# Kernel tuning notes

Hardware: AMD Instinct MI355X
Metric: run time of the kernel (lower is better)

## Reference

```python
import jax, jax.numpy as jnp
import numpy as np

B, N_IN, D_IN, N_OUT, D_OUT = 64, 2048, 16, 64, 16
GATE_EPS = 1e-6
SCALE = 1.0 / np.sqrt(D_OUT).astype(np.float32)  # 1/sqrt(out_d_capsules)


def setup_inputs() -> dict:
    key = jax.random.key(0)
    k0, k1, k2, k3, k4 = jax.random.split(key, 5)
    w_init = np.float32(np.sqrt(N_OUT / (D_IN * N_IN)))
    return {
        "input": jax.random.normal(k0, (B, N_IN, D_IN), jnp.float32),
        "current_act": jax.random.uniform(k1, (B, N_IN), jnp.float32),
        "next_capsule_value": jax.random.normal(k2, (B, N_OUT, D_OUT), jnp.float32),
        "next_act": jax.random.uniform(k3, (B, N_OUT), jnp.float32),
        "w": w_init * jax.random.normal(k4, (N_IN, D_IN, N_OUT, D_OUT), jnp.float32),
        "num_iter": 1,
    }


def reference(input, current_act, next_capsule_value, next_act, w, num_iter):
    # gate: gate_temp=1.0, gate_min=0, gate_max=1 -> reduces to clamp to [eps, 1-eps]
    act = jnp.clip(current_act, GATE_EPS, 1.0 - GATE_EPS)  # [B,N]
    # votes: shared between score and combine einsums (faithful: same contraction)
    votes = jnp.einsum('bna,namd->bnmd', input, w)  # [B,N,M,D]
    # routing logits: 'bna,namd,bmd->bnm' * scale
    scores = jnp.einsum('bnmd,bmd->bnm', votes, next_capsule_value) * SCALE
    qk = jax.nn.softmax(scores, axis=2)                       # softmax over out-capsules
    qk = qk * next_act[:, None, :]                            # 'bnm,bm->bnm'
    qk = qk / (jnp.sum(qk, axis=2, keepdims=True) + 1e-10)    # renormalize over m
    # combine: 'bnm,bna,namd,bn->bmd'
    out = jnp.einsum('bnm,bn,bnmd->bmd', qk, act, votes)      # [B,M,D]
    # act_type='EM' -> next_act passes through; dropout p=0 and identity nonlinearity
    return (out, next_act, qk)
```

## Files before the change

### kernel.cpp

```cpp
#include <hip/hip_runtime.h>
#include <stdint.h>
#include <stddef.h>

constexpr int B_ = 64, N_ = 2048, A_ = 16, M_ = 64, D_ = 16;
constexpr float SCALE_ = 0.25f;
constexpr float EPS_ = 1e-6f;

typedef float f32x4 __attribute__((ext_vector_type(4)));

#define GL16(g, l)                                                             \
  __builtin_amdgcn_global_load_lds((__attribute__((address_space(1))) void*)(g), \
                                   (__attribute__((address_space(3))) void*)(l), \
                                   16, 0, 0)

__global__ __launch_bounds__(256, 2)
void caps_main(
    const float* __restrict__ input,
    const float* __restrict__ cact,
    const float* __restrict__ ncv,
    const float* __restrict__ nact,
    const float* __restrict__ w,
    float* __restrict__ qk_out,
    float* __restrict__ partial,
    int C, int nch)
{
  __shared__ __align__(128) char wl[32768];

  const int tid  = threadIdx.x;
  const int lane = tid & 63;
  const int wv   = __builtin_amdgcn_readfirstlane(tid >> 6);

  const int flat = blockIdx.x;
  int bg, ch;
  if (nch & 7) { bg = flat & 3; ch = flat >> 2; }
  else { bg = (flat >> 3) & 3; ch = ((flat >> 5) << 3) | (flat & 7); }

  const int b0 = bg * 16 + wv * 4;
  const int n0 = ch * C;

  int offj[4];
#pragma unroll
  for (int j = 0; j < 4; ++j)
    offj[j] = (lane * 64 + j * 16) ^ (((lane >> 1) & 7) << 4);

  float na[4], cv[4][16];
#pragma unroll
  for (int bi = 0; bi < 4; ++bi) {
    na[bi] = nact[(b0 + bi) * M_ + lane];
    const f32x4* np4 = (const f32x4*)(ncv + ((size_t)(b0 + bi) * M_ + lane) * D_);
#pragma unroll
    for (int j = 0; j < 4; ++j) {
      const f32x4 t = np4[j];
      cv[bi][4*j+0] = t.x; cv[bi][4*j+1] = t.y;
      cv[bi][4*j+2] = t.z; cv[bi][4*j+3] = t.w;
    }
  }

  float acc[4][16];
#pragma unroll
  for (int bi = 0; bi < 4; ++bi)
#pragma unroll
    for (int d = 0; d < 16; ++d) acc[bi][d] = 0.f;

  for (int k = 0; k < C; ++k) {
    const int n = n0 + k;

    float v[4][16];
#pragma unroll
    for (int bi = 0; bi < 4; ++bi)
#pragma unroll
      for (int d = 0; d < 16; ++d) v[bi][d] = 0.f;

    int ibase[4];
#pragma unroll
    for (int bi = 0; bi < 4; ++bi)
      ibase[bi] = __builtin_amdgcn_readfirstlane(((b0 + bi) * N_ + n) * A_);

#pragma unroll
    for (int h = 0; h < 2; ++h) {
      {
        const char* ws = (const char*)w + ((size_t)n << 16) + ((size_t)h << 15);
#pragma unroll
        for (int i = 0; i < 8; ++i) {
          const uint32_t P = (uint32_t)(i * 4096 + tid * 16);
          const uint32_t S = P ^ (((P >> 7) & 7u) << 4);
          GL16(ws + S, (char*)wl + i * 4096 + wv * 1024);
        }
      }
      __syncthreads();

#pragma unroll
      for (int al = 0; al < 8; ++al) {
        f32x4 wr[4];
#pragma unroll
        for (int j = 0; j < 4; ++j)
          wr[j] = *(const f32x4*)((const char*)wl + al * 4096 + offj[j]);
#pragma unroll
        for (int bi = 0; bi < 4; ++bi) {
          const float x = input[ibase[bi] + h * 8 + al];
#pragma unroll
          for (int j = 0; j < 4; ++j) {
            v[bi][4*j+0] += x * wr[j].x; v[bi][4*j+1] += x * wr[j].y;
            v[bi][4*j+2] += x * wr[j].z; v[bi][4*j+3] += x * wr[j].w;
          }
        }
      }
      __syncthreads();
    }

#pragma unroll
    for (int bi = 0; bi < 4; ++bi) {
      float s = 0.f;
#pragma unroll
      for (int d = 0; d < 16; ++d) s += v[bi][d] * cv[bi][d];
      s *= SCALE_;
      const float e = __expf(s);
      const float ena = e * na[bi];
      float Ps = ena;
#pragma unroll
      for (int off = 32; off >= 1; off >>= 1) Ps += __shfl_xor(Ps, off, 64);
      const float qk = ena / Ps;
      qk_out[((size_t)(b0 + bi) * N_ + n) * M_ + lane] = qk;
      float ab = cact[__builtin_amdgcn_readfirstlane((b0 + bi) * N_ + n)];
      ab = fminf(fmaxf(ab, EPS_), 1.0f - EPS_);
      const float wq = qk * ab;
#pragma unroll
      for (int d = 0; d < 16; ++d) acc[bi][d] += wq * v[bi][d];
    }
  }

#pragma unroll
  for (int bi = 0; bi < 4; ++bi) {
    float* pp = partial + (((size_t)ch * B_ + (b0 + bi)) * M_ + lane) * D_;
#pragma unroll
    for (int j = 0; j < 4; ++j) {
      f32x4 t;
      t.x = acc[bi][4*j+0]; t.y = acc[bi][4*j+1];
      t.z = acc[bi][4*j+2]; t.w = acc[bi][4*j+3];
      __builtin_nontemporal_store(t, (f32x4*)pp + j);
    }
  }
}

__global__ void caps_reduce(const float* __restrict__ part,
                            const float* __restrict__ nain,
                            float* __restrict__ out, int nch)
{
  const int i = blockIdx.x * 256 + threadIdx.x;
  float s = 0.f;
  for (int c = 0; c < nch; ++c) s += part[(size_t)c * (B_ * M_ * D_) + i];
  out[i] = s;
  if (i < B_ * M_) out[B_ * M_ * D_ + i] = nain[i];
}

extern "C" void kernel_launch(void* const* d_in, const int* in_sizes, int n_in,
                              void* d_out, int out_size, void* d_ws, size_t ws_size,
                              hipStream_t stream)
{
  const float* input = (const float*)d_in[0];
  const float* cact  = (const float*)d_in[1];
  const float* ncv   = (const float*)d_in[2];
  const float* nact  = (const float*)d_in[3];
  const float* w     = (const float*)d_in[4];

  float* out     = (float*)d_out;
  float* qk_out  = out + (B_ * M_ * D_) + (B_ * M_);
  float* partial = (float*)d_ws;

  int nch = 256;
  while ((size_t)nch * (size_t)(B_ * M_ * D_) * sizeof(float) > ws_size && nch > 8) nch >>= 1;
  const int C = N_ / nch;

  hipLaunchKernelGGL(caps_main, dim3(4 * nch), dim3(256), 0, stream,
                     input, cact, ncv, nact, w, qk_out, partial, C, nch);
  hipLaunchKernelGGL(caps_reduce, dim3(B_ * M_ * D_ / 256), dim3(256), 0, stream,
                     partial, nact, out, nch);
}
```

Measured before the change: 217.1 us.

## Double-buffer weight tiles in LDS with manual vmcnt waits to overlap loads

Splits the weight staging into two 32KB LDS buffers. The next half-tile is issued via global_load_lds while the current one is computed, and explicit s_waitcnt vmcnt counts and barriers sequence the pipeline. Input values are now read as vectorized f32x4 loads per half instead of scalar loads inside the inner loop, and initial loads are drained up front. This roughly doubles LDS use to 64KB per block, which may limit occupancy at 2 blocks/CU, and the hand-counted vmcnt values must stay consistent with the issued loads.

```diff
diff --git a/kernel.cpp b/kernel.cpp
--- a/kernel.cpp
+++ b/kernel.cpp
@@ -12,6 +12,14 @@
   __builtin_amdgcn_global_load_lds((__attribute__((address_space(1))) void*)(g), \
                                    (__attribute__((address_space(3))) void*)(l), \
                                    16, 0, 0)
+
+#define WV(n) asm volatile("s_waitcnt vmcnt(" #n ")" ::: "memory")
+#define BAR() do {                        \
+    asm volatile("" ::: "memory");        \
+    __builtin_amdgcn_s_barrier();         \
+    asm volatile("" ::: "memory");        \
+    __builtin_amdgcn_sched_barrier(0);    \
+  } while (0)
 
 __global__ __launch_bounds__(256, 2)
 void caps_main(
@@ -24,7 +32,7 @@
     float* __restrict__ partial,
     int C, int nch)
 {
-  __shared__ __align__(128) char wl[32768];
+  __shared__ __align__(128) char wl[2][32768];
 
   const int tid  = threadIdx.x;
   const int lane = tid & 63;
@@ -55,6 +63,17 @@
       cv[bi][4*j+2] = t.z; cv[bi][4*j+3] = t.w;
     }
   }
+  {
+    float pin = 0.f;
+#pragma unroll
+    for (int bi = 0; bi < 4; ++bi) {
+      pin += na[bi];
+#pragma unroll
+      for (int d = 0; d < 16; ++d) pin += cv[bi][d];
+    }
+    asm volatile("" :: "v"(pin));
+    asm volatile("s_waitcnt vmcnt(0) lgkmcnt(0)" ::: "memory");
+  }
 
   float acc[4][16];
 #pragma unroll
@@ -62,72 +81,89 @@
 #pragma unroll
     for (int d = 0; d < 16; ++d) acc[bi][d] = 0.f;
 
-  for (int k = 0; k < C; ++k) {
-    const int n = n0 + k;
-
-    float v[4][16];
-#pragma unroll
-    for (int bi = 0; bi < 4; ++bi)
-#pragma unroll
-      for (int d = 0; d < 16; ++d) v[bi][d] = 0.f;
-
-    int ibase[4];
-#pragma unroll
-    for (int bi = 0; bi < 4; ++bi)
-      ibase[bi] = __builtin_amdgcn_readfirstlane(((b0 + bi) * N_ + n) * A_);
-
-#pragma unroll
-    for (int h = 0; h < 2; ++h) {
-      {
-        const char* ws = (const char*)w + ((size_t)n << 16) + ((size_t)h << 15);
-#pragma unroll
-        for (int i = 0; i < 8; ++i) {
-          const uint32_t P = (uint32_t)(i * 4096 + tid * 16);
-          const uint32_t S = P ^ (((P >> 7) & 7u) << 4);
-          GL16(ws + S, (char*)wl + i * 4096 + wv * 1024);
+  auto STAGE = [&](int h) {
+    const int n = n0 + (h >> 1);
+    const char* ws = (const char*)w + ((size_t)n << 16) + ((size_t)(h & 1) << 15);
+    char* lb = (char*)wl[h & 1] + wv * 1024;
+#pragma unroll
+    for (int i = 0; i < 8; ++i) {
+      const uint32_t P = (uint32_t)(i * 4096 + tid * 16);
+      const uint32_t S = P ^ (((P >> 7) & 7u) << 4);
+      GL16(ws + S, lb + i * 4096);
+    }
+  };
+
+  float v[4][16];
+
+  auto COMPUTE = [&](int h) {
+    const int n  = n0 + (h >> 1);
+    const int ah = h & 1;
+    const char* lb = (const char*)wl[ah];
+    if (ah == 0) {
+#pragma unroll
+      for (int bi = 0; bi < 4; ++bi)
+#pragma unroll
+        for (int d = 0; d < 16; ++d) v[bi][d] = 0.f;
+    }
+    float ib[4][8];
+#pragma unroll
+    for (int bi = 0; bi < 4; ++bi) {
+      const int ibase = __builtin_amdgcn_readfirstlane(
+          ((b0 + bi) * N_ + n) * A_ + ah * 8);
+      const f32x4 r0 = *(const f32x4*)(input + ibase);
+      const f32x4 r1 = *(const f32x4*)(input + ibase + 4);
+      ib[bi][0] = r0.x; ib[bi][1] = r0.y; ib[bi][2] = r0.z; ib[bi][3] = r0.w;
+      ib[bi][4] = r1.x; ib[bi][5] = r1.y; ib[bi][6] = r1.z; ib[bi][7] = r1.w;
+    }
+#pragma unroll
+    for (int al = 0; al < 8; ++al) {
+      f32x4 wr[4];
+#pragma unroll
+      for (int j = 0; j < 4; ++j)
+        wr[j] = *(const f32x4*)(lb + al * 4096 + offj[j]);
+#pragma unroll
+      for (int bi = 0; bi < 4; ++bi) {
+        const float x = ib[bi][al];
+#pragma unroll
+        for (int j = 0; j < 4; ++j) {
+          v[bi][4*j+0] += x * wr[j].x; v[bi][4*j+1] += x * wr[j].y;
+          v[bi][4*j+2] += x * wr[j].z; v[bi][4*j+3] += x * wr[j].w;
         }
       }
-      __syncthreads();
-
-#pragma unroll
-      for (int al = 0; al < 8; ++al) {
-        f32x4 wr[4];
-#pragma unroll
-        for (int j = 0; j < 4; ++j)
-          wr[j] = *(const f32x4*)((const char*)wl + al * 4096 + offj[j]);
-#pragma unroll
-        for (int bi = 0; bi < 4; ++bi) {
-          const float x = input[ibase[bi] + h * 8 + al];
-#pragma unroll
-          for (int j = 0; j < 4; ++j) {
-            v[bi][4*j+0] += x * wr[j].x; v[bi][4*j+1] += x * wr[j].y;
-            v[bi][4*j+2] += x * wr[j].z; v[bi][4*j+3] += x * wr[j].w;
-          }
-        }
+    }
+    if (ah == 1) {
+#pragma unroll
+      for (int bi = 0; bi < 4; ++bi) {
+        float s = 0.f;
+#pragma unroll
+        for (int d = 0; d < 16; ++d) s += v[bi][d] * cv[bi][d];
+        s *= SCALE_;
+        const float e = __expf(s);
+        const float ena = e * na[bi];
+        float Ps = ena;
+#pragma unroll
+        for (int off = 32; off >= 1; off >>= 1) Ps += __shfl_xor(Ps, off, 64);
+        const float qk = ena / Ps;
+        qk_out[((size_t)(b0 + bi) * N_ + n) * M_ + lane] = qk;
+        float ab = cact[__builtin_amdgcn_readfirstlane((b0 + bi) * N_ + n)];
+        ab = fminf(fmaxf(ab, EPS_), 1.0f - EPS_);
+        const float wq = qk * ab;
+#pragma unroll
+        for (int d = 0; d < 16; ++d) acc[bi][d] += wq * v[bi][d];
       }
-      __syncthreads();
-    }
-
-#pragma unroll
-    for (int bi = 0; bi < 4; ++bi) {
-      float s = 0.f;
-#pragma unroll
-      for (int d = 0; d < 16; ++d) s += v[bi][d] * cv[bi][d];
-      s *= SCALE_;
-      const float e = __expf(s);
-      const float ena = e * na[bi];
-      float Ps = ena;
-#pragma unroll
-      for (int off = 32; off >= 1; off >>= 1) Ps += __shfl_xor(Ps, off, 64);
-      const float qk = ena / Ps;
-      qk_out[((size_t)(b0 + bi) * N_ + n) * M_ + lane] = qk;
-      float ab = cact[__builtin_amdgcn_readfirstlane((b0 + bi) * N_ + n)];
-      ab = fminf(fmaxf(ab, EPS_), 1.0f - EPS_);
-      const float wq = qk * ab;
-#pragma unroll
-      for (int d = 0; d < 16; ++d) acc[bi][d] += wq * v[bi][d];
-    }
-  }
+    }
+  };
+
+  STAGE(0);
+  STAGE(1);
+  WV(8);  BAR(); COMPUTE(0); BAR(); STAGE(2);
+  WV(8);  BAR(); COMPUTE(1); BAR(); STAGE(3);
+  for (int k = 1; k < C - 1; ++k) {
+    WV(12); BAR(); COMPUTE(2 * k);     BAR(); STAGE(2 * k + 2);
+    WV(8);  BAR(); COMPUTE(2 * k + 1); BAR(); STAGE(2 * k + 3);
+  }
+  WV(12); BAR(); COMPUTE(2 * C - 2); BAR();
+  WV(0);  BAR(); COMPUTE(2 * C - 1); BAR();
 
 #pragma unroll
   for (int bi = 0; bi < 4; ++bi) {
@@ -168,7 +204,7 @@
   float* partial = (float*)d_ws;
 
   int nch = 256;
-  while ((size_t)nch * (size_t)(B_ * M_ * D_) * sizeof(float) > ws_size && nch > 8) nch >>= 1;
+  while ((size_t)nch * (size_t)(B_ * M_ * D_) * sizeof(float) > ws_size && nch > 32) nch >>= 1;
   const int C = N_ / nch;
 
   hipLaunchKernelGGL(caps_main, dim3(4 * nch), dim3(256), 0, stream,
```

Measured after the change: 486.1 us. 2.24x slower.

## Double-buffer weight tiles in LDS to overlap global loads with FMA compute

Applied to the files above, without the earlier changes.

Splits the LDS weight staging into two 32KB buffers. The next half-tile of w is issued with global_load_lds while the current half is being consumed, replacing the old serial load, barrier, compute, barrier sequence. The per-half input values are now fetched as two vector loads instead of scalar loads inside the inner loop. The minimum chunk count for the workspace fallback is also raised. LDS use per block doubles to 64KB, which may tighten occupancy at two blocks per CU.

```diff
diff --git a/kernel.cpp b/kernel.cpp
--- a/kernel.cpp
+++ b/kernel.cpp
@@ -13,6 +13,45 @@
                                    (__attribute__((address_space(3))) void*)(l), \
                                    16, 0, 0)
 
+#define STAGE(BUF, NN, HH)                                                     \
+  { const char* ws_ = (const char*)w + ((size_t)(NN) << 16) + ((size_t)(HH) << 15); \
+    char* lb_ = (char*)wl[BUF] + wv * 1024;                                    \
+    _Pragma("unroll")                                                          \
+    for (int i_ = 0; i_ < 8; ++i_) {                                           \
+      const uint32_t P_ = (uint32_t)(i_ * 4096 + tid * 16);                    \
+      const uint32_t S_ = P_ ^ (((P_ >> 7) & 7u) << 4);                        \
+      GL16(ws_ + S_, lb_ + i_ * 4096);                                         \
+    } }
+
+#define COMPUTE_HALF(BUF, NN, HH)                                              \
+  { const char* lb_ = (const char*)wl[BUF];                                    \
+    float ib_[4][8];                                                           \
+    _Pragma("unroll")                                                          \
+    for (int bi = 0; bi < 4; ++bi) {                                           \
+      const int ibase_ = __builtin_amdgcn_readfirstlane(                       \
+          ((b0 + bi) * N_ + (NN)) * A_ + (HH) * 8);                            \
+      const f32x4 r0_ = *(const f32x4*)(input + ibase_);                       \
+      const f32x4 r1_ = *(const f32x4*)(input + ibase_ + 4);                   \
+      ib_[bi][0] = r0_.x; ib_[bi][1] = r0_.y; ib_[bi][2] = r0_.z; ib_[bi][3] = r0_.w; \
+      ib_[bi][4] = r1_.x; ib_[bi][5] = r1_.y; ib_[bi][6] = r1_.z; ib_[bi][7] = r1_.w; \
+    }                                                                          \
+    _Pragma("unroll")                                                          \
+    for (int al = 0; al < 8; ++al) {                                           \
+      f32x4 wr_[4];                                                            \
+      _Pragma("unroll")                                                        \
+      for (int j = 0; j < 4; ++j)                                              \
+        wr_[j] = *(const f32x4*)(lb_ + al * 4096 + offj[j]);                   \
+      _Pragma("unroll")                                                        \
+      for (int bi = 0; bi < 4; ++bi) {                                         \
+        const float x_ = ib_[bi][al];                                          \
+        _Pragma("unroll")                                                      \
+        for (int j = 0; j < 4; ++j) {                                          \
+          v[bi][4*j+0] += x_ * wr_[j].x; v[bi][4*j+1] += x_ * wr_[j].y;        \
+          v[bi][4*j+2] += x_ * wr_[j].z; v[bi][4*j+3] += x_ * wr_[j].w;        \
+        }                                                                      \
+      }                                                                        \
+    } }
+
 __global__ __launch_bounds__(256, 2)
 void caps_main(
     const float* __restrict__ input,
@@ -24,7 +63,7 @@
     float* __restrict__ partial,
     int C, int nch)
 {
-  __shared__ __align__(128) char wl[32768];
+  __shared__ __align__(128) char wl[2][32768];
 
   const int tid  = threadIdx.x;
   const int lane = tid & 63;
@@ -62,6 +101,9 @@
 #pragma unroll
     for (int d = 0; d < 16; ++d) acc[bi][d] = 0.f;
 
+  STAGE(0, n0, 0);
+  __syncthreads();
+
   for (int k = 0; k < C; ++k) {
     const int n = n0 + k;
 
@@ -71,42 +113,12 @@
 #pragma unroll
       for (int d = 0; d < 16; ++d) v[bi][d] = 0.f;
 
-    int ibase[4];
-#pragma unroll
-    for (int bi = 0; bi < 4; ++bi)
-      ibase[bi] = __builtin_amdgcn_readfirstlane(((b0 + bi) * N_ + n) * A_);
+    STAGE(1, n, 1);
+    COMPUTE_HALF(0, n, 0);
+    __syncthreads();
 
-#pragma unroll
-    for (int h = 0; h < 2; ++h) {
-      {
-        const char* ws = (const char*)w + ((size_t)n << 16) + ((size_t)h << 15);
-#pragma unroll
-        for (int i = 0; i < 8; ++i) {
-          const uint32_t P = (uint32_t)(i * 4096 + tid * 16);
-          const uint32_t S = P ^ (((P >> 7) & 7u) << 4);
-          GL16(ws + S, (char*)wl + i * 4096 + wv * 1024);
-        }
-      }
-      __syncthreads();
-
-#pragma unroll
-      for (int al = 0; al < 8; ++al) {
-        f32x4 wr[4];
-#pragma unroll
-        for (int j = 0; j < 4; ++j)
-          wr[j] = *(const f32x4*)((const char*)wl + al * 4096 + offj[j]);
-#pragma unroll
-        for (int bi = 0; bi < 4; ++bi) {
-          const float x = input[ibase[bi] + h * 8 + al];
-#pragma unroll
-          for (int j = 0; j < 4; ++j) {
-            v[bi][4*j+0] += x * wr[j].x; v[bi][4*j+1] += x * wr[j].y;
-            v[bi][4*j+2] += x * wr[j].z; v[bi][4*j+3] += x * wr[j].w;
-          }
-        }
-      }
-      __syncthreads();
-    }
+    if (k + 1 < C) { STAGE(0, n + 1, 0); }
+    COMPUTE_HALF(1, n, 1);
 
 #pragma unroll
     for (int bi = 0; bi < 4; ++bi) {
@@ -127,6 +139,8 @@
 #pragma unroll
       for (int d = 0; d < 16; ++d) acc[bi][d] += wq * v[bi][d];
     }
+
+    __syncthreads();
   }
 
 #pragma unroll
@@ -168,7 +182,7 @@
   float* partial = (float*)d_ws;
 
   int nch = 256;
-  while ((size_t)nch * (size_t)(B_ * M_ * D_) * sizeof(float) > ws_size && nch > 8) nch >>= 1;
+  while ((size_t)nch * (size_t)(B_ * M_ * D_) * sizeof(float) > ws_size && nch > 32) nch >>= 1;
   const int C = N_ / nch;
 
   hipLaunchKernelGGL(caps_main, dim3(4 * nch), dim3(256), 0, stream,
```

Result: slower. 374.3 us (+72.4%).
